# Kernel optimization log

Hardware: AMD Instinct MI355X
Metric: run time of the kernel (lower is better)

## Reference

```python
import jax, jax.numpy as jnp
import numpy as np

N_NODES = 100000
N_EDGES = 300000
N_GRAPHS = 4096
EMB = 256
L = 5
EPS = 1e-5


def setup_inputs() -> dict:
    key = jax.random.key(0)
    ks = jax.random.split(key, 16)
    x = jax.random.normal(ks[0], (N_NODES, 40), dtype=jnp.float32)
    edge_index = jax.random.randint(ks[1], (2, N_EDGES), 0, N_NODES, dtype=jnp.int32)
    edge_attr = jax.random.normal(ks[2], (N_EDGES, 10), dtype=jnp.float32)
    batch = jnp.sort(jax.random.randint(ks[3], (N_NODES,), 0, N_GRAPHS, dtype=jnp.int32))
    s = lambda fan: 1.0 / np.sqrt(fan)
    params = {
        "x_emb_W": jax.random.normal(ks[4], (EMB, 40), jnp.float32) * np.sqrt(2.0 / 40),
        "x_emb_b": jnp.zeros((EMB,), jnp.float32),
        "e_emb_W": jax.random.normal(ks[5], (EMB, 10), jnp.float32) * np.sqrt(2.0 / 10),
        "e_emb_b": jnp.zeros((EMB,), jnp.float32),
        "gcn_W": jax.random.normal(ks[6], (L, EMB, EMB), jnp.float32) * s(EMB),
        "gcn_b": jax.random.normal(ks[7], (L, EMB), jnp.float32) * s(EMB),
        "root_emb": jax.random.normal(ks[8], (L, EMB), jnp.float32),
        "bn_gamma": jnp.ones((L, EMB), jnp.float32),
        "bn_beta": jnp.zeros((L, EMB), jnp.float32),
        "p1_W": jax.random.normal(ks[9], (EMB // 2, EMB), jnp.float32) * s(EMB),
        "p1_b": jnp.zeros((EMB // 2,), jnp.float32),
        "p2_W": jax.random.normal(ks[10], (EMB // 2, EMB // 2), jnp.float32) * s(EMB // 2),
        "p2_b": jnp.zeros((EMB // 2,), jnp.float32),
        "p3_W": jax.random.normal(ks[11], (1, EMB // 2), jnp.float32) * s(EMB // 2),
        "p3_b": jnp.zeros((1,), jnp.float32),
    }
    return dict(x=x, edge_index=edge_index, edge_attr=edge_attr, batch=batch, **params)


def _gcn_conv(h, row, col, ea, W, b, root):
    # h: [N, D] node feats; ea: [E, D] edge feats
    hx = h @ W.T + b
    deg = jax.ops.segment_sum(jnp.ones_like(row, dtype=hx.dtype), row, num_segments=N_NODES) + 1.0
    dinv = deg ** -0.5
    norm = dinv[row] * dinv[col]                      # [E]
    msg = norm[:, None] * jax.nn.relu(hx[row] + ea)   # gather + relu + scale
    agg = jax.ops.segment_sum(msg, col, num_segments=N_NODES)  # scatter-add to targets
    return agg + jax.nn.relu(hx + root) / deg[:, None]


def _batchnorm(h, gamma, beta):
    mean = jnp.mean(h, axis=0)
    var = jnp.var(h, axis=0)
    return (h - mean) * jax.lax.rsqrt(var + EPS) * gamma + beta


def reference(x, edge_index, edge_attr, batch,
              x_emb_W, x_emb_b, e_emb_W, e_emb_b,
              gcn_W, gcn_b, root_emb, bn_gamma, bn_beta,
              p1_W, p1_b, p2_W, p2_b, p3_W, p3_b):
    row, col = edge_index[0], edge_index[1]
    h = x @ x_emb_W.T + x_emb_b
    ea = edge_attr @ e_emb_W.T + e_emb_b
    for l in range(L):
        h_in = h
        h = _gcn_conv(h, row, col, ea, gcn_W[l], gcn_b[l], root_emb[l])
        h = _batchnorm(h_in + h, bn_gamma[l], bn_beta[l])
        if l != L - 1:
            h = jax.nn.relu(h)
        # dropout is identity in eval mode
    # global mean pool over graphs
    sums = jax.ops.segment_sum(h, batch, num_segments=N_GRAPHS)
    cnts = jax.ops.segment_sum(jnp.ones((h.shape[0],), h.dtype), batch, num_segments=N_GRAPHS)
    g = sums / jnp.maximum(cnts, 1.0)[:, None]
    # prediction head: Lin-ReLU-Lin-ReLU-Lin
    g = jax.nn.relu(g @ p1_W.T + p1_b)
    g = jax.nn.relu(g @ p2_W.T + p2_b)
    return g @ p3_W.T + p3_b
```

## Files before the change

### kernel.cpp

```cpp
#include <hip/hip_runtime.h>
#include <hip/hip_bf16.h>

#define NN 100000
#define NE 300000
#define NG 4096
#define EMB 256
#define NLAYERS 5

typedef unsigned short u16;
typedef unsigned int u32;

typedef short bf16x8 __attribute__((ext_vector_type(8)));
typedef float f32x4 __attribute__((ext_vector_type(4)));

__device__ __forceinline__ float b2f(u16 u){
    union { float f; u32 i; } v; v.i = ((u32)u) << 16; return v.f;
}
__device__ __forceinline__ u16 f2b(float f){
    __hip_bfloat16 h = __float2bfloat16(f);
    union { __hip_bfloat16 h; u16 u; } v; v.h = h; return v.u;
}
__device__ __forceinline__ void bnsc_f(const float* __restrict__ stats,
        const float* __restrict__ gamma, const float* __restrict__ beta,
        int f, float& sc, float& sh)
{
    const float inv = 1.0f / (float)NN;
    float mean = stats[f] * inv;
    float var  = stats[256+f] * inv - mean*mean;
    float is = rsqrtf(var + 1e-5f);
    sc = gamma[f] * is;
    sh = fmaf(-mean, sc, beta[f]);
}

#define XNB 32
__global__ __launch_bounds__(256) void embed_x(const float* __restrict__ x,
        const float* __restrict__ W, const float* __restrict__ b,
        u16* __restrict__ t)
{
    __shared__ float sW[256][41];
    __shared__ float sx[XNB][40];
    int tid = threadIdx.x;
    for (int i = tid; i < 256*40; i += 256) sW[i/40][i%40] = W[i];
    int n0 = blockIdx.x * XNB;
    for (int i = tid; i < XNB*40; i += 256) {
        int j = i/40, k = i%40;
        sx[j][k] = x[(size_t)(n0+j)*40 + k];
    }
    __syncthreads();
    float bb = b[tid];
    for (int j = 0; j < XNB; ++j) {
        float a = bb;
        #pragma unroll
        for (int k = 0; k < 40; ++k) a = fmaf(sW[tid][k], sx[j][k], a);
        t[(size_t)(n0+j)*EMB + tid] = f2b(a);
    }
}

__global__ void wconv(const float* __restrict__ W, u16* __restrict__ Wb, int n)
{
    int i = blockIdx.x*256 + threadIdx.x;
    if (i < n) Wb[i] = f2b(W[i]);
}

__global__ void ewt_kernel(const float* __restrict__ eW, float* __restrict__ eWt)
{
    int i = blockIdx.x*256 + threadIdx.x;
    if (i < 2560) { int f = i/10, k = i%10; eWt[k*256 + f] = eW[i]; }
}

__global__ void hist_kernel(const int* __restrict__ row, const int* __restrict__ col,
        int* __restrict__ rcnt, int* __restrict__ ccnt, int E)
{
    int e = blockIdx.x*256 + threadIdx.x;
    if (e < E) {
        atomicAdd(&rcnt[row[e]], 1);
        atomicAdd(&ccnt[col[e]], 1);
    }
}

__global__ void deg_fin(const int* __restrict__ rcnt, float* __restrict__ dinv,
                        float* __restrict__ invdg, int N)
{
    int n = blockIdx.x*256 + threadIdx.x;
    if (n < N) {
        float d = (float)rcnt[n] + 1.0f;
        dinv[n]  = rsqrtf(d);
        invdg[n] = 1.0f/d;
    }
}

__global__ void scan1(const int* __restrict__ cnt, int* __restrict__ bsum, int N)
{
    __shared__ int sh[256];
    int t = threadIdx.x, i = blockIdx.x*256 + t;
    sh[t] = (i < N) ? cnt[i] : 0;
    __syncthreads();
    for (int off = 128; off > 0; off >>= 1) {
        if (t < off) sh[t] += sh[t+off];
        __syncthreads();
    }
    if (t == 0) bsum[blockIdx.x] = sh[0];
}

__global__ __launch_bounds__(512) void scan2(const int* __restrict__ bsum,
        int* __restrict__ bbase, int* __restrict__ coff, int nb)
{
    __shared__ int a[512], b[512];
    int t = threadIdx.x;
    a[t] = (t < nb) ? bsum[t] : 0;
    __syncthreads();
    int* src = a; int* dst = b;
    for (int off = 1; off < 512; off <<= 1) {
        dst[t] = (t >= off) ? src[t-off] + src[t] : src[t];
        __syncthreads();
        int* tmp = src; src = dst; dst = tmp;
    }
    bbase[t] = t ? src[t-1] : 0;
    if (t == 0) coff[NN] = NE;
}

__global__ void scan3(const int* __restrict__ cnt, const int* __restrict__ bbase,
        int* __restrict__ coff, int N)
{
    __shared__ int a[256], b[256];
    int t = threadIdx.x, i = blockIdx.x*256 + t;
    a[t] = (i < N) ? cnt[i] : 0;
    __syncthreads();
    int* src = a; int* dst = b;
    for (int off = 1; off < 256; off <<= 1) {
        dst[t] = (t >= off) ? src[t-off] + src[t] : src[t];
        __syncthreads();
        int* tmp = src; src = dst; dst = tmp;
    }
    if (i < N) coff[i] = bbase[blockIdx.x] + (t ? src[t-1] : 0);
}

__global__ void csr_fill(const int* __restrict__ row, const int* __restrict__ col,
        const float* __restrict__ eattr, const int* __restrict__ coff,
        const float* __restrict__ dinv, int* __restrict__ fill,
        int2* __restrict__ epack, u16* __restrict__ eab, int E)
{
    int e = blockIdx.x*256 + threadIdx.x;
    if (e < E) {
        int c = col[e], r = row[e];
        int p = coff[c] + atomicAdd(&fill[c], 1);
        int2 ep; ep.x = r; ep.y = __float_as_int(dinv[r] * dinv[c]);
        epack[p] = ep;
        #pragma unroll
        for (int k = 0; k < 10; ++k) eab[(size_t)p*16 + k] = f2b(eattr[(size_t)e*10 + k]);
        #pragma unroll
        for (int k = 10; k < 16; ++k) eab[(size_t)p*16 + k] = 0;
    }
}

#define CS_STRIDE 144
__global__ __launch_bounds__(512) void gemm_mfma(const u16* __restrict__ A,
        const u16* __restrict__ Wb, const float* __restrict__ bias,
        const float* __restrict__ stats, const float* __restrict__ gamma,
        const float* __restrict__ beta, int doBN,
        u16* __restrict__ C, int M)
{
    __shared__ __align__(16) char smem[38912];
    u16* As = (u16*)smem;
    float* scS = (float*)(smem + 36864);
    float* shS = scS + 256;
    const int tid = threadIdx.x;
    if (doBN && tid < 256) {
        float s, h; bnsc_f(stats, gamma, beta, tid, s, h);
        scS[tid] = s; shS[tid] = h;
    }
    const int wid  = tid >> 6;
    const int lane = tid & 63;
    const int wm = wid >> 2, wn = wid & 3;
    const int m0 = blockIdx.x * 128;
    const int r8 = tid >> 3;
    const int ch = tid & 7;
    const int sw = ch ^ (r8 & 7);
    const int ga0 = min(m0 + r8,      M-1);
    const int ga1 = min(m0 + r8 + 64, M-1);

    uint4 ra0, ra1;
    #define LOADK(k0) do {                                                     \
        ra0 = *reinterpret_cast<const uint4*>(&A[(size_t)ga0*256 + (k0) + ch*8]); \
        ra1 = *reinterpret_cast<const uint4*>(&A[(size_t)ga1*256 + (k0) + ch*8]); \
    } while(0)

    LOADK(0);
    if (doBN) __syncthreads();
    f32x4 acc[4][4] = {};
    const int c = lane >> 4;
    const int rl = lane & 15;
    const int nb0 = wn*64 + rl;
    for (int k0 = 0; k0 < 256; k0 += 64) {
        uint4 va0 = ra0, va1 = ra1;
        if (doBN) {
            int kk = k0 + ch*8;
            u32 w0[4] = {va0.x, va0.y, va0.z, va0.w};
            u32 w1[4] = {va1.x, va1.y, va1.z, va1.w};
            #pragma unroll
            for (int j = 0; j < 4; ++j) {
                float l0 = b2f((u16)(w0[j] & 0xffffu)), h0 = b2f((u16)(w0[j] >> 16));
                float l1 = b2f((u16)(w1[j] & 0xffffu)), h1 = b2f((u16)(w1[j] >> 16));
                float s0 = scS[kk+2*j], s1 = scS[kk+2*j+1];
                float b0 = shS[kk+2*j], b1 = shS[kk+2*j+1];
                l0 = fmaxf(fmaf(l0, s0, b0), 0.f); h0 = fmaxf(fmaf(h0, s1, b1), 0.f);
                l1 = fmaxf(fmaf(l1, s0, b0), 0.f); h1 = fmaxf(fmaf(h1, s1, b1), 0.f);
                w0[j] = (u32)f2b(l0) | ((u32)f2b(h0) << 16);
                w1[j] = (u32)f2b(l1) | ((u32)f2b(h1) << 16);
            }
            va0.x=w0[0]; va0.y=w0[1]; va0.z=w0[2]; va0.w=w0[3];
            va1.x=w1[0]; va1.y=w1[1]; va1.z=w1[2]; va1.w=w1[3];
        }
        *reinterpret_cast<uint4*>(&As[((r8     )*8 + sw)*8]) = va0;
        *reinterpret_cast<uint4*>(&As[((r8 + 64)*8 + sw)*8]) = va1;
        __syncthreads();
        if (k0 < 192) LOADK(k0 + 64);
        #pragma unroll
        for (int kt = 0; kt < 2; ++kt) {
            bf16x8 af[4], bfr[4];
            #pragma unroll
            for (int f = 0; f < 4; ++f) {
                bfr[f] = *reinterpret_cast<const bf16x8*>(
                    &Wb[(size_t)(nb0 + f*16)*256 + k0 + (kt*4 + c)*8]);
                int rA = wm*64 + f*16 + rl;
                int cha = (kt*4 + c) ^ (rA & 7);
                af[f] = *reinterpret_cast<const bf16x8*>(&As[(rA*8 + cha)*8]);
            }
            #pragma unroll
            for (int fm = 0; fm < 4; ++fm)
                #pragma unroll
                for (int fn = 0; fn < 4; ++fn)
                    acc[fm][fn] = __builtin_amdgcn_mfma_f32_16x16x32_bf16(
                        af[fm], bfr[fn], acc[fm][fn], 0, 0, 0);
        }
        __syncthreads();
    }
    #undef LOADK

    u16* Cs = (u16*)smem;
    const int cn = lane & 15, rq = lane >> 4;
    #pragma unroll
    for (int pp = 0; pp < 2; ++pp) {
        if ((wn >> 1) == pp) {
            int cl0 = (wn & 1)*64;
            #pragma unroll
            for (int fn = 0; fn < 4; ++fn) {
                int n = wn*64 + fn*16 + cn;
                float bb = bias[n];
                #pragma unroll
                for (int fm = 0; fm < 4; ++fm) {
                    int rbase = wm*64 + fm*16 + rq*4;
                    #pragma unroll
                    for (int r = 0; r < 4; ++r)
                        Cs[(rbase + r)*CS_STRIDE + cl0 + fn*16 + cn] =
                            f2b(acc[fm][fn][r] + bb);
                }
            }
        }
        __syncthreads();
        #pragma unroll
        for (int it = 0; it < 4; ++it) {
            int idx = tid + it*512;
            int rowi = idx >> 4;
            int c8  = (idx & 15) * 8;
            int m = m0 + rowi;
            if (m < M)
                *reinterpret_cast<uint4*>(&C[(size_t)m*256 + pp*128 + c8]) =
                    *reinterpret_cast<const uint4*>(&Cs[rowi*CS_STRIDE + c8]);
        }
        __syncthreads();
    }
}

#define GFB 4
#define NGROUPS (NN/GFB)
__global__ __launch_bounds__(256) void gather_combine_w(const int2* __restrict__ epack,
        const u16* __restrict__ eab, const int* __restrict__ coff,
        const float* __restrict__ eWt, const float* __restrict__ ebv,
        const u16* __restrict__ hx, const float* __restrict__ rootv,
        const float* __restrict__ invdg, const float* __restrict__ statsPrev,
        const float* __restrict__ gammaPrev, const float* __restrict__ betaPrev,
        int doBN, u16* __restrict__ t, float* __restrict__ stats, int N)
{
    __shared__ float red[4][512];
    const int wid = threadIdx.x >> 6, lane = threadIdx.x & 63;
    const int f4 = lane*4;
    float w[4][10], bb[4];
    #pragma unroll
    for (int k = 0; k < 10; ++k) {
        float4 wv = *reinterpret_cast<const float4*>(&eWt[k*256 + f4]);
        w[0][k] = wv.x; w[1][k] = wv.y; w[2][k] = wv.z; w[3][k] = wv.w;
    }
    { float4 bv = *reinterpret_cast<const float4*>(&ebv[f4]);
      bb[0]=bv.x; bb[1]=bv.y; bb[2]=bv.z; bb[3]=bv.w; }
    float4 root = *reinterpret_cast<const float4*>(&rootv[f4]);
    float sc[4] = {1,1,1,1}, sh[4] = {0,0,0,0};
    if (doBN) {
        #pragma unroll
        for (int j = 0; j < 4; ++j)
            bnsc_f(statsPrev, gammaPrev, betaPrev, f4+j, sc[j], sh[j]);
    }
    float sacc[4] = {0,0,0,0}, s2acc[4] = {0,0,0,0};

    for (int g = blockIdx.x*4 + wid; g < NGROUPS; g += gridDim.x*4) {
        const int nb = g*GFB;
        int c1 = coff[nb+1], c2 = coff[nb+2], c3 = coff[nb+3], c4 = coff[nb+4];
        int s = coff[nb], e = c4;
        int jn = 0, cend = c1;
        float acc[4] = {0,0,0,0};

        #define FLUSH() do {                                                   \
            int n_ = nb + jn;                                                  \
            size_t idx_ = (size_t)n_*EMB + f4;                                 \
            uint2 hv_ = *reinterpret_cast<const uint2*>(&t[idx_]);             \
            uint2 xv_ = *reinterpret_cast<const uint2*>(&hx[idx_]);            \
            float id_ = invdg[n_];                                             \
            float hh_[4] = { b2f((u16)(hv_.x&0xffffu)), b2f((u16)(hv_.x>>16)), \
                             b2f((u16)(hv_.y&0xffffu)), b2f((u16)(hv_.y>>16)) };\
            float xx_[4] = { b2f((u16)(xv_.x&0xffffu)), b2f((u16)(xv_.x>>16)), \
                             b2f((u16)(xv_.y&0xffffu)), b2f((u16)(xv_.y>>16)) };\
            float rt_[4] = { root.x, root.y, root.z, root.w };                 \
            u16 ov_[4];                                                        \
            _Pragma("unroll")                                                  \
            for (int jj = 0; jj < 4; ++jj) {                                   \
                float hin_ = hh_[jj];                                          \
                if (doBN) hin_ = fmaxf(fmaf(hin_, sc[jj], sh[jj]), 0.f);       \
                float rv_ = xx_[jj] + rt_[jj];                                 \
                rv_ = rv_ > 0.f ? rv_ : 0.f;                                   \
                float tv_ = hin_ + acc[jj] + rv_*id_;                          \
                ov_[jj] = f2b(tv_);                                            \
                sacc[jj] += tv_; s2acc[jj] += tv_*tv_;                         \
                acc[jj] = 0.f;                                                 \
            }                                                                  \
            uint2 o_; o_.x = (u32)ov_[0] | ((u32)ov_[1]<<16);                  \
            o_.y = (u32)ov_[2] | ((u32)ov_[3]<<16);                            \
            *reinterpret_cast<uint2*>(&t[idx_]) = o_;                          \
            ++jn; cend = (jn==1) ? c2 : (jn==2) ? c3 : c4;                     \
        } while(0)

        #define CONSUME(nm, hvv, alo, ahi) do {                                \
            float hf_[4] = { b2f((u16)((hvv).x&0xffffu)), b2f((u16)((hvv).x>>16)),\
                             b2f((u16)((hvv).y&0xffffu)), b2f((u16)((hvv).y>>16)) };\
            float at_[10];                                                     \
            at_[0]=b2f((u16)((alo).x&0xffffu)); at_[1]=b2f((u16)((alo).x>>16));\
            at_[2]=b2f((u16)((alo).y&0xffffu)); at_[3]=b2f((u16)((alo).y>>16));\
            at_[4]=b2f((u16)((alo).z&0xffffu)); at_[5]=b2f((u16)((alo).z>>16));\
            at_[6]=b2f((u16)((alo).w&0xffffu)); at_[7]=b2f((u16)((alo).w>>16));\
            at_[8]=b2f((u16)((ahi).x&0xffffu)); at_[9]=b2f((u16)((ahi).x>>16));\
            _Pragma("unroll")                                                  \
            for (int jj = 0; jj < 4; ++jj) {                                   \
                float ea_ = bb[jj];                                            \
                _Pragma("unroll")                                              \
                for (int k = 0; k < 10; ++k) ea_ = fmaf(at_[k], w[jj][k], ea_);\
                float v_ = hf_[jj] + ea_;                                      \
                acc[jj] += v_ > 0.f ? v_*(nm) : 0.f;                           \
            }                                                                  \
        } while(0)

        int p = s;
        for (; p + 4 <= e; p += 4) {
            int2 e0 = epack[p], e1 = epack[p+1], e2 = epack[p+2], e3 = epack[p+3];
            uint2 h0 = *reinterpret_cast<const uint2*>(&hx[(size_t)e0.x*EMB + f4]);
            uint2 h1 = *reinterpret_cast<const uint2*>(&hx[(size_t)e1.x*EMB + f4]);
            uint2 h2 = *reinterpret_cast<const uint2*>(&hx[(size_t)e2.x*EMB + f4]);
            uint2 h3 = *reinterpret_cast<const uint2*>(&hx[(size_t)e3.x*EMB + f4]);
            uint4 a0l = *reinterpret_cast<const uint4*>(&eab[(size_t)(p+0)*16]);
            uint4 a0h = *reinterpret_cast<const uint4*>(&eab[(size_t)(p+0)*16+8]);
            uint4 a1l = *reinterpret_cast<const uint4*>(&eab[(size_t)(p+1)*16]);
            uint4 a1h = *reinterpret_cast<const uint4*>(&eab[(size_t)(p+1)*16+8]);
            uint4 a2l = *reinterpret_cast<const uint4*>(&eab[(size_t)(p+2)*16]);
            uint4 a2h = *reinterpret_cast<const uint4*>(&eab[(size_t)(p+2)*16+8]);
            uint4 a3l = *reinterpret_cast<const uint4*>(&eab[(size_t)(p+3)*16]);
            uint4 a3h = *reinterpret_cast<const uint4*>(&eab[(size_t)(p+3)*16+8]);
            while (p+0 >= cend) FLUSH();
            CONSUME(__int_as_float(e0.y), h0, a0l, a0h);
            while (p+1 >= cend) FLUSH();
            CONSUME(__int_as_float(e1.y), h1, a1l, a1h);
            while (p+2 >= cend) FLUSH();
            CONSUME(__int_as_float(e2.y), h2, a2l, a2h);
            while (p+3 >= cend) FLUSH();
            CONSUME(__int_as_float(e3.y), h3, a3l, a3h);
        }
        for (; p < e; ++p) {
            int2 e0 = epack[p];
            uint2 h0 = *reinterpret_cast<const uint2*>(&hx[(size_t)e0.x*EMB + f4]);
            uint4 a0l = *reinterpret_cast<const uint4*>(&eab[(size_t)p*16]);
            uint4 a0h = *reinterpret_cast<const uint4*>(&eab[(size_t)p*16+8]);
            while (p >= cend) FLUSH();
            CONSUME(__int_as_float(e0.y), h0, a0l, a0h);
        }
        while (jn < GFB) FLUSH();
        #undef FLUSH
        #undef CONSUME
    }

    #pragma unroll
    for (int j = 0; j < 4; ++j) {
        red[wid][f4+j]     = sacc[j];
        red[wid][256+f4+j] = s2acc[j];
    }
    __syncthreads();
    int tt = threadIdx.x;
    float a0 = red[0][tt] + red[1][tt] + red[2][tt] + red[3][tt];
    float a1 = red[0][256+tt] + red[1][256+tt] + red[2][256+tt] + red[3][256+tt];
    atomicAdd(&stats[tt], a0);
    atomicAdd(&stats[256+tt], a1);
}

__global__ __launch_bounds__(256) void pool_kernel(const u16* __restrict__ t,
        const int* __restrict__ batch, const float* __restrict__ stats5,
        const float* __restrict__ gamma5, const float* __restrict__ beta5,
        float* __restrict__ psum, float* __restrict__ pcnt, int N)
{
    int tid = threadIdx.x;
    int half = tid >> 7;
    int pp = tid & 127;
    const u32* t32 = (const u32*)t;
    float sc0, sh0, sc1, sh1;
    bnsc_f(stats5, gamma5, beta5, 2*pp,   sc0, sh0);
    bnsc_f(stats5, gamma5, beta5, 2*pp+1, sc1, sh1);
    int n0 = blockIdx.x * 256;
    int n1 = min(n0 + 256, N);
    int start = n0 + half;
    if (start >= n1) return;
    int cur = batch[start];
    float a0 = 0.f, a1 = 0.f;
    int cnt = 0;
    for (int n = start; n < n1; n += 2) {
        int gb = batch[n];
        if (gb != cur) {
            atomicAdd(&psum[(size_t)cur*EMB + 2*pp],   a0);
            atomicAdd(&psum[(size_t)cur*EMB + 2*pp+1], a1);
            if (pp == 0) atomicAdd(&pcnt[cur], (float)cnt);
            a0 = a1 = 0.f; cnt = 0; cur = gb;
        }
        u32 v = t32[(size_t)n*128 + pp];
        a0 += fmaf(b2f((u16)(v & 0xffffu)), sc0, sh0);
        a1 += fmaf(b2f((u16)(v >> 16)),     sc1, sh1);
        ++cnt;
    }
    atomicAdd(&psum[(size_t)cur*EMB + 2*pp],   a0);
    atomicAdd(&psum[(size_t)cur*EMB + 2*pp+1], a1);
    if (pp == 0) atomicAdd(&pcnt[cur], (float)cnt);
}

__global__ void pool2g(const float* __restrict__ psum, const float* __restrict__ pcnt,
        u16* __restrict__ gbf)
{
    int i = blockIdx.x*256 + threadIdx.x;
    if (i < NG*128) {
        int g = i >> 7, p2 = (i & 127)*2;
        float invc = 1.0f / fmaxf(pcnt[g], 1.0f);
        u32 pk = (u32)f2b(psum[(size_t)g*EMB + p2] * invc)
               | ((u32)f2b(psum[(size_t)g*EMB + p2 + 1] * invc) << 16);
        ((u32*)gbf)[i] = pk;
    }
}

__global__ __launch_bounds__(256) void gemm_head(const u16* __restrict__ A,
        const u16* __restrict__ W, const float* __restrict__ bias,
        u16* __restrict__ C, int M, int K)
{
    __shared__ u16 As[128*64];
    __shared__ u16 Bs[128*64];
    const int tid  = threadIdx.x;
    const int wid  = tid >> 6;
    const int lane = tid & 63;
    const int wr = wid >> 1, wc = wid & 1;
    const int m0 = blockIdx.x * 128;
    f32x4 acc[4][4] = {};
    for (int k0 = 0; k0 < K; k0 += 64) {
        #pragma unroll
        for (int i = 0; i < 4; ++i) {
            int L = tid + i*256;
            int rowi = L >> 3, ch = L & 7;
            int sw = ch ^ (rowi & 7);
            int gr = m0 + rowi; gr = gr < M ? gr : M-1;
            uint4 va = *reinterpret_cast<const uint4*>(&A[(size_t)gr*K + k0 + ch*8]);
            *reinterpret_cast<uint4*>(&As[(rowi*8 + sw)*8]) = va;
            uint4 vb = *reinterpret_cast<const uint4*>(&W[(size_t)rowi*K + k0 + ch*8]);
            *reinterpret_cast<uint4*>(&Bs[(rowi*8 + sw)*8]) = vb;
        }
        __syncthreads();
        const int c = lane >> 4;
        const int rl = lane & 15;
        #pragma unroll
        for (int kt = 0; kt < 2; ++kt) {
            bf16x8 af[4], bfr[4];
            #pragma unroll
            for (int f = 0; f < 4; ++f) {
                int ra = wr*64 + f*16 + rl;
                int cha = (kt*4 + c) ^ (ra & 7);
                af[f] = *reinterpret_cast<const bf16x8*>(&As[(ra*8 + cha)*8]);
                int rb = wc*64 + f*16 + rl;
                int chb = (kt*4 + c) ^ (rb & 7);
                bfr[f] = *reinterpret_cast<const bf16x8*>(&Bs[(rb*8 + chb)*8]);
            }
            #pragma unroll
            for (int fm = 0; fm < 4; ++fm)
                #pragma unroll
                for (int fn = 0; fn < 4; ++fn)
                    acc[fm][fn] = __builtin_amdgcn_mfma_f32_16x16x32_bf16(
                        af[fm], bfr[fn], acc[fm][fn], 0, 0, 0);
        }
        __syncthreads();
    }
    const int cn = lane & 15, rq = lane >> 4;
    #pragma unroll
    for (int fn = 0; fn < 4; ++fn) {
        int n = wc*64 + fn*16 + cn;
        float bb = bias[n];
        #pragma unroll
        for (int fm = 0; fm < 4; ++fm) {
            #pragma unroll
            for (int r = 0; r < 4; ++r) {
                int m = m0 + wr*64 + fm*16 + rq*4 + r;
                if (m < M) C[(size_t)m*128 + n] = f2b(fmaxf(acc[fm][fn][r] + bb, 0.f));
            }
        }
    }
}

__global__ __launch_bounds__(256) void head_final(const u16* __restrict__ h2,
        const float* __restrict__ p3W, const float* __restrict__ p3b,
        float* __restrict__ out, int G)
{
    int tid = blockIdx.x*256 + threadIdx.x;
    int g = tid >> 4, sub = tid & 15;
    if (g >= G) return;
    uint4 v = *reinterpret_cast<const uint4*>(&h2[(size_t)g*128 + sub*8]);
    u32 wv[4] = {v.x, v.y, v.z, v.w};
    float s = 0.f;
    #pragma unroll
    for (int j = 0; j < 4; ++j) {
        s = fmaf(b2f((u16)(wv[j] & 0xffffu)), p3W[sub*8 + 2*j],   s);
        s = fmaf(b2f((u16)(wv[j] >> 16)),     p3W[sub*8 + 2*j+1], s);
    }
    s += __shfl_down(s, 8, 16);
    s += __shfl_down(s, 4, 16);
    s += __shfl_down(s, 2, 16);
    s += __shfl_down(s, 1, 16);
    if (sub == 0) out[g] = s + p3b[0];
}

extern "C" void kernel_launch(void* const* d_in, const int* in_sizes, int n_in,
                              void* d_out, int out_size, void* d_ws, size_t ws_size,
                              hipStream_t stream)
{
    const float* x     = (const float*)d_in[0];
    const int*   eidx  = (const int*)d_in[1];
    const float* eattr = (const float*)d_in[2];
    const int*   batch = (const int*)d_in[3];
    const float* xW    = (const float*)d_in[4];
    const float* xb    = (const float*)d_in[5];
    const float* eW    = (const float*)d_in[6];
    const float* eb    = (const float*)d_in[7];
    const float* gcnW  = (const float*)d_in[8];
    const float* gcnb  = (const float*)d_in[9];
    const float* rootE = (const float*)d_in[10];
    const float* bng   = (const float*)d_in[11];
    const float* bnb   = (const float*)d_in[12];
    const float* p1W   = (const float*)d_in[13];
    const float* p1b   = (const float*)d_in[14];
    const float* p2W   = (const float*)d_in[15];
    const float* p2b   = (const float*)d_in[16];
    const float* p3W   = (const float*)d_in[17];
    const float* p3b   = (const float*)d_in[18];
    float* out = (float*)d_out;

    const int* row = eidx;
    const int* col = eidx + NE;

    const size_t HSZ = (size_t)NN * EMB;
    const int NWB = 5*EMB*EMB;

    char* p = (char*)d_ws;
    u16* t   = (u16*)p;            p += HSZ*2;
    u16* hx  = (u16*)p;            p += HSZ*2;
    u16* Wb  = (u16*)p;            p += (size_t)NWB*2;
    float* eWt = (float*)p;        p += 2560*4;
    char* zbase = p;
    int* rcnt   = (int*)p;         p += (size_t)NN*4;
    int* ccnt   = (int*)p;         p += (size_t)NN*4;
    int* fill   = (int*)p;         p += (size_t)NN*4;
    float* stats= (float*)p;       p += (size_t)NLAYERS*512*4;
    float* psum = (float*)p;       p += (size_t)NG*EMB*4;
    float* pcnt = (float*)p;       p += (size_t)NG*4;
    size_t zbytes = (size_t)(p - zbase);
    float* dinv = (float*)p;       p += (size_t)NN*4;
    float* invdg= (float*)p;       p += (size_t)NN*4;
    int* coff   = (int*)p;         p += (size_t)(NN+1)*4;
    int* bsum   = (int*)p;         p += 512*4;
    int* bbase  = (int*)p;         p += 512*4;
    int2* epack = (int2*)p;        p += (size_t)NE*8;
    u16* eab    = (u16*)p;         p += (size_t)NE*16*2;
    u16* gbf    = (u16*)p;         p += (size_t)NG*EMB*2;
    u16* h1b    = (u16*)p;         p += (size_t)NG*128*2;
    u16* h2b    = (u16*)p;         p += (size_t)NG*128*2;
    u16* Wh1    = (u16*)p;         p += (size_t)128*256*2;
    u16* Wh2    = (u16*)p;         p += (size_t)128*128*2;
    size_t NEED = (size_t)(p - (char*)d_ws);
    if (ws_size < NEED) return;

    hipMemsetAsync(zbase, 0, zbytes, stream);

    const int NBS = (NN + 255)/256;

    embed_x<<<NN/XNB, 256, 0, stream>>>(x, xW, xb, t);
    wconv<<<(NWB+255)/256, 256, 0, stream>>>(gcnW, Wb, NWB);
    wconv<<<(128*256+255)/256, 256, 0, stream>>>(p1W, Wh1, 128*256);
    wconv<<<(128*128+255)/256, 256, 0, stream>>>(p2W, Wh2, 128*128);
    ewt_kernel<<<10, 256, 0, stream>>>(eW, eWt);
    hist_kernel<<<(NE+255)/256, 256, 0, stream>>>(row, col, rcnt, ccnt, NE);
    deg_fin<<<NBS, 256, 0, stream>>>(rcnt, dinv, invdg, NN);
    scan1<<<NBS, 256, 0, stream>>>(ccnt, bsum, NN);
    scan2<<<1, 512, 0, stream>>>(bsum, bbase, coff, NBS);
    scan3<<<NBS, 256, 0, stream>>>(ccnt, bbase, coff, NN);
    csr_fill<<<(NE+255)/256, 256, 0, stream>>>(row, col, eattr, coff, dinv, fill,
                                               epack, eab, NE);

    for (int l = 0; l < NLAYERS; ++l) {
        const u16*   Wl = Wb + (size_t)l*EMB*EMB;
        const float* bl = gcnb + (size_t)l*EMB;
        const float* rl = rootE + (size_t)l*EMB;
        const float* stPrev = stats + (size_t)(l > 0 ? l-1 : 0)*512;
        const float* gmPrev = bng + (size_t)(l > 0 ? l-1 : 0)*EMB;
        const float* btPrev = bnb + (size_t)(l > 0 ? l-1 : 0)*EMB;
        int doBN = (l > 0) ? 1 : 0;
        gemm_mfma<<<(NN+127)/128, 512, 0, stream>>>(t, Wl, bl, stPrev, gmPrev,
                                                    btPrev, doBN, hx, NN);
        gather_combine_w<<<1536, 256, 0, stream>>>(epack, eab, coff, eWt, eb,
                hx, rl, invdg, stPrev, gmPrev, btPrev, doBN, t, stats + l*512, NN);
    }

    pool_kernel<<<NBS, 256, 0, stream>>>(t, batch, stats + (size_t)(NLAYERS-1)*512,
            bng + (size_t)(NLAYERS-1)*EMB, bnb + (size_t)(NLAYERS-1)*EMB,
            psum, pcnt, NN);
    pool2g<<<(NG*128+255)/256, 256, 0, stream>>>(psum, pcnt, gbf);
    gemm_head<<<NG/128, 256, 0, stream>>>(gbf, Wh1, p1b, h1b, NG, 256);
    gemm_head<<<NG/128, 256, 0, stream>>>(h1b, Wh2, p2b, h2b, NG, 128);
    head_final<<<(NG*16+255)/256, 256, 0, stream>>>(h2b, p3W, p3b, out, NG);
}
```

Measured before the change: 944.7 us.

## Double-buffer GEMM LDS tiles and fuse mean-pool into final gather layer

The node GEMM now uses two LDS buffers so staging the next K-slice overlaps MFMA work on the current one, with one barrier per step instead of two, and launch bounds request higher occupancy. The last-layer gather kernel no longer writes bf16 node features; it atomically adds fp32 pre-BN values straight into per-graph sums. The final batchnorm affine is applied after averaging in pool2g, which is valid because it is linear. This removes the separate pool kernel and one full feature write plus read, but adds per-node global atomics, which may contend.

Measured after the change: 1.170 ms. 1.24x slower.

```diff
diff --git a/kernel.cpp b/kernel.cpp
--- a/kernel.cpp
+++ b/kernel.cpp
@@ -154,14 +154,15 @@
 }
 
 #define CS_STRIDE 144
-__global__ __launch_bounds__(512) void gemm_mfma(const u16* __restrict__ A,
+__global__ __launch_bounds__(512, 4) void gemm_mfma(const u16* __restrict__ A,
         const u16* __restrict__ Wb, const float* __restrict__ bias,
         const float* __restrict__ stats, const float* __restrict__ gamma,
         const float* __restrict__ beta, int doBN,
         u16* __restrict__ C, int M)
 {
     __shared__ __align__(16) char smem[38912];
-    u16* As = (u16*)smem;
+    u16* As0 = (u16*)smem;
+    u16* As1 = (u16*)(smem + 16384);
     float* scS = (float*)(smem + 36864);
     float* shS = scS + 256;
     const int tid = threadIdx.x;
@@ -178,6 +179,9 @@
     const int sw = ch ^ (r8 & 7);
     const int ga0 = min(m0 + r8,      M-1);
     const int ga1 = min(m0 + r8 + 64, M-1);
+    const int c  = lane >> 4;
+    const int rl = lane & 15;
+    const int nb0 = wn*64 + rl;
 
     uint4 ra0, ra1;
     #define LOADK(k0) do {                                                     \
@@ -185,57 +189,71 @@
         ra1 = *reinterpret_cast<const uint4*>(&A[(size_t)ga1*256 + (k0) + ch*8]); \
     } while(0)
 
+    #define STAGE(dst, k0v) do {                                               \
+        uint4 va0 = ra0, va1 = ra1;                                            \
+        if (doBN) {                                                            \
+            int kk = (k0v) + ch*8;                                             \
+            u32 w0[4] = {va0.x, va0.y, va0.z, va0.w};                          \
+            u32 w1[4] = {va1.x, va1.y, va1.z, va1.w};                          \
+            _Pragma("unroll")                                                  \
+            for (int j = 0; j < 4; ++j) {                                      \
+                float l0 = b2f((u16)(w0[j] & 0xffffu)), h0 = b2f((u16)(w0[j] >> 16)); \
+                float l1 = b2f((u16)(w1[j] & 0xffffu)), h1 = b2f((u16)(w1[j] >> 16)); \
+                float s0 = scS[kk+2*j], s1 = scS[kk+2*j+1];                    \
+                float b0 = shS[kk+2*j], b1 = shS[kk+2*j+1];                    \
+                l0 = fmaxf(fmaf(l0, s0, b0), 0.f); h0 = fmaxf(fmaf(h0, s1, b1), 0.f); \
+                l1 = fmaxf(fmaf(l1, s0, b0), 0.f); h1 = fmaxf(fmaf(h1, s1, b1), 0.f); \
+                w0[j] = (u32)f2b(l0) | ((u32)f2b(h0) << 16);                   \
+                w1[j] = (u32)f2b(l1) | ((u32)f2b(h1) << 16);                   \
+            }                                                                  \
+            va0.x=w0[0]; va0.y=w0[1]; va0.z=w0[2]; va0.w=w0[3];                \
+            va1.x=w1[0]; va1.y=w1[1]; va1.z=w1[2]; va1.w=w1[3];                \
+        }                                                                      \
+        *reinterpret_cast<uint4*>(&(dst)[((r8     )*8 + sw)*8]) = va0;         \
+        *reinterpret_cast<uint4*>(&(dst)[((r8 + 64)*8 + sw)*8]) = va1;         \
+    } while(0)
+
+    f32x4 acc[4][4] = {};
+    #define KSTEP(cur, k0v) do {                                               \
+        _Pragma("unroll")                                                      \
+        for (int kt = 0; kt < 2; ++kt) {                                       \
+            bf16x8 af[4], bfr[4];                                              \
+            _Pragma("unroll")                                                  \
+            for (int f = 0; f < 4; ++f) {                                      \
+                bfr[f] = *reinterpret_cast<const bf16x8*>(                     \
+                    &Wb[(size_t)(nb0 + f*16)*256 + (k0v) + (kt*4 + c)*8]);     \
+                int rA = wm*64 + f*16 + rl;                                    \
+                int cha = (kt*4 + c) ^ (rA & 7);                               \
+                af[f] = *reinterpret_cast<const bf16x8*>(&(cur)[(rA*8 + cha)*8]); \
+            }                                                                  \
+            _Pragma("unroll")                                                  \
+            for (int fm = 0; fm < 4; ++fm)                                     \
+                _Pragma("unroll")                                              \
+                for (int fn = 0; fn < 4; ++fn)                                 \
+                    acc[fm][fn] = __builtin_amdgcn_mfma_f32_16x16x32_bf16(     \
+                        af[fm], bfr[fn], acc[fm][fn], 0, 0, 0);                \
+        }                                                                      \
+    } while(0)
+
     LOADK(0);
     if (doBN) __syncthreads();
-    f32x4 acc[4][4] = {};
-    const int c = lane >> 4;
-    const int rl = lane & 15;
-    const int nb0 = wn*64 + rl;
-    for (int k0 = 0; k0 < 256; k0 += 64) {
-        uint4 va0 = ra0, va1 = ra1;
-        if (doBN) {
-            int kk = k0 + ch*8;
-            u32 w0[4] = {va0.x, va0.y, va0.z, va0.w};
-            u32 w1[4] = {va1.x, va1.y, va1.z, va1.w};
-            #pragma unroll
-            for (int j = 0; j < 4; ++j) {
-                float l0 = b2f((u16)(w0[j] & 0xffffu)), h0 = b2f((u16)(w0[j] >> 16));
-                float l1 = b2f((u16)(w1[j] & 0xffffu)), h1 = b2f((u16)(w1[j] >> 16));
-                float s0 = scS[kk+2*j], s1 = scS[kk+2*j+1];
-                float b0 = shS[kk+2*j], b1 = shS[kk+2*j+1];
-                l0 = fmaxf(fmaf(l0, s0, b0), 0.f); h0 = fmaxf(fmaf(h0, s1, b1), 0.f);
-                l1 = fmaxf(fmaf(l1, s0, b0), 0.f); h1 = fmaxf(fmaf(h1, s1, b1), 0.f);
-                w0[j] = (u32)f2b(l0) | ((u32)f2b(h0) << 16);
-                w1[j] = (u32)f2b(l1) | ((u32)f2b(h1) << 16);
-            }
-            va0.x=w0[0]; va0.y=w0[1]; va0.z=w0[2]; va0.w=w0[3];
-            va1.x=w1[0]; va1.y=w1[1]; va1.z=w1[2]; va1.w=w1[3];
-        }
-        *reinterpret_cast<uint4*>(&As[((r8     )*8 + sw)*8]) = va0;
-        *reinterpret_cast<uint4*>(&As[((r8 + 64)*8 + sw)*8]) = va1;
-        __syncthreads();
-        if (k0 < 192) LOADK(k0 + 64);
-        #pragma unroll
-        for (int kt = 0; kt < 2; ++kt) {
-            bf16x8 af[4], bfr[4];
-            #pragma unroll
-            for (int f = 0; f < 4; ++f) {
-                bfr[f] = *reinterpret_cast<const bf16x8*>(
-                    &Wb[(size_t)(nb0 + f*16)*256 + k0 + (kt*4 + c)*8]);
-                int rA = wm*64 + f*16 + rl;
-                int cha = (kt*4 + c) ^ (rA & 7);
-                af[f] = *reinterpret_cast<const bf16x8*>(&As[(rA*8 + cha)*8]);
-            }
-            #pragma unroll
-            for (int fm = 0; fm < 4; ++fm)
-                #pragma unroll
-                for (int fn = 0; fn < 4; ++fn)
-                    acc[fm][fn] = __builtin_amdgcn_mfma_f32_16x16x32_bf16(
-                        af[fm], bfr[fn], acc[fm][fn], 0, 0, 0);
-        }
-        __syncthreads();
-    }
+    STAGE(As0, 0);
+    LOADK(64);
+    __syncthreads();
+    STAGE(As1, 64); LOADK(128);
+    KSTEP(As0, 0);
+    __syncthreads();
+    STAGE(As0, 128); LOADK(192);
+    KSTEP(As1, 64);
+    __syncthreads();
+    STAGE(As1, 192);
+    KSTEP(As0, 128);
+    __syncthreads();
+    KSTEP(As1, 192);
+    __syncthreads();
     #undef LOADK
+    #undef STAGE
+    #undef KSTEP
 
     u16* Cs = (u16*)smem;
     const int cn = lane & 15, rq = lane >> 4;
@@ -274,13 +292,16 @@
 
 #define GFB 4
 #define NGROUPS (NN/GFB)
-__global__ __launch_bounds__(256) void gather_combine_w(const int2* __restrict__ epack,
+template<int LAST>
+__global__ __launch_bounds__(256) void gather_combine_t(const int2* __restrict__ epack,
         const u16* __restrict__ eab, const int* __restrict__ coff,
         const float* __restrict__ eWt, const float* __restrict__ ebv,
         const u16* __restrict__ hx, const float* __restrict__ rootv,
         const float* __restrict__ invdg, const float* __restrict__ statsPrev,
         const float* __restrict__ gammaPrev, const float* __restrict__ betaPrev,
-        int doBN, u16* __restrict__ t, float* __restrict__ stats, int N)
+        int doBN, u16* __restrict__ t, float* __restrict__ stats,
+        const int* __restrict__ batch, float* __restrict__ psum,
+        float* __restrict__ pcnt, int N)
 {
     __shared__ float red[4][512];
     const int wid = threadIdx.x >> 6, lane = threadIdx.x & 63;
@@ -320,7 +341,7 @@
             float xx_[4] = { b2f((u16)(xv_.x&0xffffu)), b2f((u16)(xv_.x>>16)), \
                              b2f((u16)(xv_.y&0xffffu)), b2f((u16)(xv_.y>>16)) };\
             float rt_[4] = { root.x, root.y, root.z, root.w };                 \
-            u16 ov_[4];                                                        \
+            float tvv_[4];                                                     \
             _Pragma("unroll")                                                  \
             for (int jj = 0; jj < 4; ++jj) {                                   \
                 float hin_ = hh_[jj];                                          \
@@ -328,13 +349,24 @@
                 float rv_ = xx_[jj] + rt_[jj];                                 \
                 rv_ = rv_ > 0.f ? rv_ : 0.f;                                   \
                 float tv_ = hin_ + acc[jj] + rv_*id_;                          \
-                ov_[jj] = f2b(tv_);                                            \
+                tvv_[jj] = tv_;                                                \
                 sacc[jj] += tv_; s2acc[jj] += tv_*tv_;                         \
                 acc[jj] = 0.f;                                                 \
             }                                                                  \
-            uint2 o_; o_.x = (u32)ov_[0] | ((u32)ov_[1]<<16);                  \
-            o_.y = (u32)ov_[2] | ((u32)ov_[3]<<16);                            \
-            *reinterpret_cast<uint2*>(&t[idx_]) = o_;                          \
+            if (!LAST) {                                                       \
+                uint2 o_;                                                      \
+                o_.x = (u32)f2b(tvv_[0]) | ((u32)f2b(tvv_[1])<<16);            \
+                o_.y = (u32)f2b(tvv_[2]) | ((u32)f2b(tvv_[3])<<16);            \
+                *reinterpret_cast<uint2*>(&t[idx_]) = o_;                      \
+            } else {                                                           \
+                int gb_ = batch[n_];                                           \
+                float* ps_ = &psum[(size_t)gb_*EMB + f4];                      \
+                atomicAdd(&ps_[0], tvv_[0]);                                   \
+                atomicAdd(&ps_[1], tvv_[1]);                                   \
+                atomicAdd(&ps_[2], tvv_[2]);                                   \
+                atomicAdd(&ps_[3], tvv_[3]);                                   \
+                if (f4 == 0) atomicAdd(&pcnt[gb_], 1.0f);                      \
+            }                                                                  \
             ++jn; cend = (jn==1) ? c2 : (jn==2) ? c3 : c4;                     \
         } while(0)
 
@@ -407,52 +439,24 @@
     atomicAdd(&stats[256+tt], a1);
 }
 
-__global__ __launch_bounds__(256) void pool_kernel(const u16* __restrict__ t,
-        const int* __restrict__ batch, const float* __restrict__ stats5,
-        const float* __restrict__ gamma5, const float* __restrict__ beta5,
-        float* __restrict__ psum, float* __restrict__ pcnt, int N)
-{
-    int tid = threadIdx.x;
-    int half = tid >> 7;
-    int pp = tid & 127;
-    const u32* t32 = (const u32*)t;
-    float sc0, sh0, sc1, sh1;
-    bnsc_f(stats5, gamma5, beta5, 2*pp,   sc0, sh0);
-    bnsc_f(stats5, gamma5, beta5, 2*pp+1, sc1, sh1);
-    int n0 = blockIdx.x * 256;
-    int n1 = min(n0 + 256, N);
-    int start = n0 + half;
-    if (start >= n1) return;
-    int cur = batch[start];
-    float a0 = 0.f, a1 = 0.f;
-    int cnt = 0;
-    for (int n = start; n < n1; n += 2) {
-        int gb = batch[n];
-        if (gb != cur) {
-            atomicAdd(&psum[(size_t)cur*EMB + 2*pp],   a0);
-            atomicAdd(&psum[(size_t)cur*EMB + 2*pp+1], a1);
-            if (pp == 0) atomicAdd(&pcnt[cur], (float)cnt);
-            a0 = a1 = 0.f; cnt = 0; cur = gb;
-        }
-        u32 v = t32[(size_t)n*128 + pp];
-        a0 += fmaf(b2f((u16)(v & 0xffffu)), sc0, sh0);
-        a1 += fmaf(b2f((u16)(v >> 16)),     sc1, sh1);
-        ++cnt;
-    }
-    atomicAdd(&psum[(size_t)cur*EMB + 2*pp],   a0);
-    atomicAdd(&psum[(size_t)cur*EMB + 2*pp+1], a1);
-    if (pp == 0) atomicAdd(&pcnt[cur], (float)cnt);
-}
-
 __global__ void pool2g(const float* __restrict__ psum, const float* __restrict__ pcnt,
-        u16* __restrict__ gbf)
+        const float* __restrict__ stats5, const float* __restrict__ gamma5,
+        const float* __restrict__ beta5, u16* __restrict__ gbf)
 {
     int i = blockIdx.x*256 + threadIdx.x;
     if (i < NG*128) {
         int g = i >> 7, p2 = (i & 127)*2;
-        float invc = 1.0f / fmaxf(pcnt[g], 1.0f);
-        u32 pk = (u32)f2b(psum[(size_t)g*EMB + p2] * invc)
-               | ((u32)f2b(psum[(size_t)g*EMB + p2 + 1] * invc) << 16);
+        float cnt = pcnt[g];
+        float g0 = 0.f, g1 = 0.f;
+        if (cnt > 0.f) {
+            float invc = 1.0f / cnt;
+            float sc0, sh0, sc1, sh1;
+            bnsc_f(stats5, gamma5, beta5, p2,   sc0, sh0);
+            bnsc_f(stats5, gamma5, beta5, p2+1, sc1, sh1);
+            g0 = fmaf(psum[(size_t)g*EMB + p2]   * invc, sc0, sh0);
+            g1 = fmaf(psum[(size_t)g*EMB + p2+1] * invc, sc1, sh1);
+        }
+        u32 pk = (u32)f2b(g0) | ((u32)f2b(g1) << 16);
         ((u32*)gbf)[i] = pk;
     }
 }
@@ -629,14 +633,19 @@
         int doBN = (l > 0) ? 1 : 0;
         gemm_mfma<<<(NN+127)/128, 512, 0, stream>>>(t, Wl, bl, stPrev, gmPrev,
                                                     btPrev, doBN, hx, NN);
-        gather_combine_w<<<1536, 256, 0, stream>>>(epack, eab, coff, eWt, eb,
-                hx, rl, invdg, stPrev, gmPrev, btPrev, doBN, t, stats + l*512, NN);
-    }
-
-    pool_kernel<<<NBS, 256, 0, stream>>>(t, batch, stats + (size_t)(NLAYERS-1)*512,
-            bng + (size_t)(NLAYERS-1)*EMB, bnb + (size_t)(NLAYERS-1)*EMB,
-            psum, pcnt, NN);
-    pool2g<<<(NG*128+255)/256, 256, 0, stream>>>(psum, pcnt, gbf);
+        if (l < NLAYERS-1)
+            gather_combine_t<0><<<1536, 256, 0, stream>>>(epack, eab, coff, eWt, eb,
+                    hx, rl, invdg, stPrev, gmPrev, btPrev, doBN, t, stats + l*512,
+                    batch, psum, pcnt, NN);
+        else
+            gather_combine_t<1><<<1536, 256, 0, stream>>>(epack, eab, coff, eWt, eb,
+                    hx, rl, invdg, stPrev, gmPrev, btPrev, doBN, t, stats + l*512,
+                    batch, psum, pcnt, NN);
+    }
+
+    pool2g<<<(NG*128+255)/256, 256, 0, stream>>>(psum, pcnt,
+            stats + (size_t)(NLAYERS-1)*512, bng + (size_t)(NLAYERS-1)*EMB,
+            bnb + (size_t)(NLAYERS-1)*EMB, gbf);
     gemm_head<<<NG/128, 256, 0, stream>>>(gbf, Wh1, p1b, h1b, NG, 256);
     gemm_head<<<NG/128, 256, 0, stream>>>(h1b, Wh2, p2b, h2b, NG, 128);
     head_final<<<(NG*16+255)/256, 256, 0, stream>>>(h2b, p3W, p3b, out, NG);
```

## Load GEMM A fragments directly from global instead of staging through LDS

Applied to the files above, without the earlier changes.

The GEMM no longer stages the A tile through shared memory with register prefetch and per-step barriers. Each wave now loads its A and B fragments straight from global memory (relying on cache) and applies the BatchNorm affine+ReLU per fragment, using a packed bf16 convert instruction. Launch bounds request 4 blocks per SM. This removes LDS round-trips and barriers, but A rows are now read redundantly by the 4 column waves, and the global-load latency is no longer prefetched, which risks stalls.

New measurement: 1.040 ms. 10.0% more time.

```diff
diff --git a/kernel.cpp b/kernel.cpp
--- a/kernel.cpp
+++ b/kernel.cpp
@@ -30,6 +30,24 @@
     float is = rsqrtf(var + 1e-5f);
     sc = gamma[f] * is;
     sh = fmaf(-mean, sc, beta[f]);
+}
+
+__device__ __forceinline__ bf16x8 affine8(bf16x8 v, const float* __restrict__ scS,
+        const float* __restrict__ shS, int kk)
+{
+    union { bf16x8 b; u32 u[4]; } in, out;
+    in.b = v;
+    #pragma unroll
+    for (int j = 0; j < 4; ++j) {
+        float lo = __uint_as_float(in.u[j] << 16);
+        float hi = __uint_as_float(in.u[j] & 0xffff0000u);
+        lo = fmaxf(fmaf(lo, scS[kk+2*j],   shS[kk+2*j]),   0.f);
+        hi = fmaxf(fmaf(hi, scS[kk+2*j+1], shS[kk+2*j+1]), 0.f);
+        u32 r;
+        asm("v_cvt_pk_bf16_f32 %0, %1, %2" : "=v"(r) : "v"(lo), "v"(hi));
+        out.u[j] = r;
+    }
+    return out.b;
 }
 
 #define XNB 32
@@ -154,77 +172,56 @@
 }
 
 #define CS_STRIDE 144
-__global__ __launch_bounds__(512) void gemm_mfma(const u16* __restrict__ A,
+__global__ __launch_bounds__(512, 4) void gemm_mfma(const u16* __restrict__ A,
         const u16* __restrict__ Wb, const float* __restrict__ bias,
         const float* __restrict__ stats, const float* __restrict__ gamma,
         const float* __restrict__ beta, int doBN,
         u16* __restrict__ C, int M)
 {
     __shared__ __align__(16) char smem[38912];
-    u16* As = (u16*)smem;
     float* scS = (float*)(smem + 36864);
     float* shS = scS + 256;
     const int tid = threadIdx.x;
-    if (doBN && tid < 256) {
-        float s, h; bnsc_f(stats, gamma, beta, tid, s, h);
-        scS[tid] = s; shS[tid] = h;
+    if (doBN) {
+        if (tid < 256) {
+            float s, h; bnsc_f(stats, gamma, beta, tid, s, h);
+            scS[tid] = s; shS[tid] = h;
+        }
+        __syncthreads();
     }
     const int wid  = tid >> 6;
     const int lane = tid & 63;
     const int wm = wid >> 2, wn = wid & 3;
     const int m0 = blockIdx.x * 128;
-    const int r8 = tid >> 3;
-    const int ch = tid & 7;
-    const int sw = ch ^ (r8 & 7);
-    const int ga0 = min(m0 + r8,      M-1);
-    const int ga1 = min(m0 + r8 + 64, M-1);
-
-    uint4 ra0, ra1;
-    #define LOADK(k0) do {                                                     \
-        ra0 = *reinterpret_cast<const uint4*>(&A[(size_t)ga0*256 + (k0) + ch*8]); \
-        ra1 = *reinterpret_cast<const uint4*>(&A[(size_t)ga1*256 + (k0) + ch*8]); \
-    } while(0)
-
-    LOADK(0);
-    if (doBN) __syncthreads();
-    f32x4 acc[4][4] = {};
-    const int c = lane >> 4;
+    const int c  = lane >> 4;
     const int rl = lane & 15;
     const int nb0 = wn*64 + rl;
-    for (int k0 = 0; k0 < 256; k0 += 64) {
-        uint4 va0 = ra0, va1 = ra1;
-        if (doBN) {
-            int kk = k0 + ch*8;
-            u32 w0[4] = {va0.x, va0.y, va0.z, va0.w};
-            u32 w1[4] = {va1.x, va1.y, va1.z, va1.w};
-            #pragma unroll
-            for (int j = 0; j < 4; ++j) {
-                float l0 = b2f((u16)(w0[j] & 0xffffu)), h0 = b2f((u16)(w0[j] >> 16));
-                float l1 = b2f((u16)(w1[j] & 0xffffu)), h1 = b2f((u16)(w1[j] >> 16));
-                float s0 = scS[kk+2*j], s1 = scS[kk+2*j+1];
-                float b0 = shS[kk+2*j], b1 = shS[kk+2*j+1];
-                l0 = fmaxf(fmaf(l0, s0, b0), 0.f); h0 = fmaxf(fmaf(h0, s1, b1), 0.f);
-                l1 = fmaxf(fmaf(l1, s0, b0), 0.f); h1 = fmaxf(fmaf(h1, s1, b1), 0.f);
-                w0[j] = (u32)f2b(l0) | ((u32)f2b(h0) << 16);
-                w1[j] = (u32)f2b(l1) | ((u32)f2b(h1) << 16);
-            }
-            va0.x=w0[0]; va0.y=w0[1]; va0.z=w0[2]; va0.w=w0[3];
-            va1.x=w1[0]; va1.y=w1[1]; va1.z=w1[2]; va1.w=w1[3];
-        }
-        *reinterpret_cast<uint4*>(&As[((r8     )*8 + sw)*8]) = va0;
-        *reinterpret_cast<uint4*>(&As[((r8 + 64)*8 + sw)*8]) = va1;
-        __syncthreads();
-        if (k0 < 192) LOADK(k0 + 64);
+
+    const u16* aB[4];
+    const u16* bB[4];
+    #pragma unroll
+    for (int f = 0; f < 4; ++f) {
+        int rA = m0 + wm*64 + f*16 + rl;
+        rA = rA < M ? rA : M-1;
+        aB[f] = A + (size_t)rA*256;
+        bB[f] = Wb + (size_t)(nb0 + f*16)*256;
+    }
+
+    f32x4 acc[4][4] = {};
+    for (int s = 0; s < 4; ++s) {
+        const int k0 = s*64;
         #pragma unroll
         for (int kt = 0; kt < 2; ++kt) {
+            const int kc = k0 + (kt*4 + c)*8;
             bf16x8 af[4], bfr[4];
             #pragma unroll
             for (int f = 0; f < 4; ++f) {
-                bfr[f] = *reinterpret_cast<const bf16x8*>(
-                    &Wb[(size_t)(nb0 + f*16)*256 + k0 + (kt*4 + c)*8]);
-                int rA = wm*64 + f*16 + rl;
-                int cha = (kt*4 + c) ^ (rA & 7);
-                af[f] = *reinterpret_cast<const bf16x8*>(&As[(rA*8 + cha)*8]);
+                af[f]  = *reinterpret_cast<const bf16x8*>(aB[f] + kc);
+                bfr[f] = *reinterpret_cast<const bf16x8*>(bB[f] + kc);
+            }
+            if (doBN) {
+                #pragma unroll
+                for (int f = 0; f < 4; ++f) af[f] = affine8(af[f], scS, shS, kc);
             }
             #pragma unroll
             for (int fm = 0; fm < 4; ++fm)
@@ -233,10 +230,9 @@
                     acc[fm][fn] = __builtin_amdgcn_mfma_f32_16x16x32_bf16(
                         af[fm], bfr[fn], acc[fm][fn], 0, 0, 0);
         }
-        __syncthreads();
-    }
-    #undef LOADK
-
+    }
+
+    __syncthreads();
     u16* Cs = (u16*)smem;
     const int cn = lane & 15, rq = lane >> 4;
     #pragma unroll
```
